# Optimization experiments

Measured on AMD Instinct MI355X. Metric: run time of the kernel, lower is better.

Reference implementation:

```python
import jax, jax.numpy as jnp
import numpy as np
import math

B, C, H, W, T, NH, SS = 4, 64, 32, 32, 32, 8, 512


def _alibi_slopes(heads):
    def pow2(n):
        start = 2 ** (-2 ** (-(math.log2(n) - 3)))
        return [start * start ** i for i in range(n)]
    if math.log2(heads).is_integer():
        return pow2(heads)
    cp = 2 ** math.floor(math.log2(heads))
    return pow2(cp) + pow2(2 * cp)[0::2][: heads - cp]


def _style_conv(x, style, weight, lw, lb, noise_p, bias_p, noise):
    # x: (b,c,h,w,t); weight: (out,in,1,1,1) -> modulated 1x1x1 grouped conv
    s = style @ lw.T + lb                                   # (b, in)
    w = weight[None] * s[:, None, :, None, None, None]       # (b,out,in,1,1,1)
    sigma_inv = jax.lax.rsqrt(jnp.sum(w * w, axis=(2, 3, 4, 5), keepdims=True) + 1e-8)
    w = (w * sigma_inv)[:, :, :, 0, 0, 0]                    # (b,out,in)
    y = jnp.einsum('bchwt,boc->bohwt', x, w)
    y = y + noise_p * noise                                  # (out,1,1,1)*(b,1,h,w,t)
    return y + bias_p


def setup_inputs() -> dict:
    key = jax.random.key(0)
    ks = jax.random.split(key, 8)
    return {
        'x': jax.random.normal(ks[0], (B, C, H, W, T), jnp.float32),
        'style': jax.random.normal(ks[1], (B, SS), jnp.float32),
        'qkv_w': jax.random.normal(ks[2], (3 * C, C, 1, 1, 1), jnp.float32),
        'qkv_lw': jax.random.normal(ks[3], (C, SS), jnp.float32) * 0.02,
        'qkv_lb': jnp.zeros((C,), jnp.float32),
        'qkv_np': jnp.zeros((3 * C, 1, 1, 1), jnp.float32),
        'qkv_bp': jnp.zeros((3 * C, 1, 1, 1), jnp.float32),
        'qkv_noise': jax.random.normal(ks[4], (B, 1, H, W, T), jnp.float32),
        'proj_w': jax.random.normal(ks[5], (C, C, 1, 1, 1), jnp.float32),
        'proj_lw': jax.random.normal(ks[6], (C, SS), jnp.float32) * 0.02,
        'proj_lb': jnp.zeros((C,), jnp.float32),
        'proj_np': jnp.zeros((C, 1, 1, 1), jnp.float32),
        'proj_bp': jnp.zeros((C, 1, 1, 1), jnp.float32),
        'proj_noise': jax.random.normal(ks[7], (B, 1, H, W, T), jnp.float32),
    }


def reference(x, style, qkv_w, qkv_lw, qkv_lb, qkv_np, qkv_bp, qkv_noise,
              proj_w, proj_lw, proj_lb, proj_np, proj_bp, proj_noise):
    b, c, h, w, t = x.shape
    qkv = _style_conv(x, style, qkv_w, qkv_lw, qkv_lb, qkv_np, qkv_bp, qkv_noise)
    q, k, v = jnp.split(qkv, 3, axis=1)                      # each (b,c,h,w,t)

    def to_heads(z):
        z = z.reshape(b, c * h * w, t).transpose(0, 2, 1)    # (b,t,chw)
        return z.reshape(b, t, NH, (c * h * w) // NH).transpose(0, 2, 1, 3)
    q, k, v = to_heads(q), to_heads(k), to_heads(v)          # (b,nh,t,dh)
    dh = q.shape[-1]

    attn = jnp.einsum('bnid,bnjd->bnij', q, k) / math.sqrt(dh)
    slopes = jnp.asarray(_alibi_slopes(NH), dtype=attn.dtype)[:, None, None]
    pos = -jnp.abs(jnp.arange(t)[None, :] - jnp.arange(t)[:, None]).astype(attn.dtype)
    attn = attn + slopes * pos                                # ALiBi bias
    # Faithful to original: masked_fill where tril(ones) is True (lower triangle masked)
    mask = jnp.tril(jnp.ones((t, t), bool))
    attn = jnp.where(mask, jnp.asarray(-1e18, attn.dtype), attn)
    attn = jax.nn.softmax(attn, axis=-1)
    out = jnp.einsum('bnij,bnjd->bnid', attn, v)              # (b,nh,t,dh)

    out = out.transpose(0, 2, 1, 3).reshape(b, t, c * h * w)  # (b,t,chw)
    out = out.reshape(b, t, c, h, w).transpose(0, 2, 3, 4, 1) # (b,c,h,w,t)
    return _style_conv(out, style, proj_w, proj_lw, proj_lb, proj_np, proj_bp, proj_noise)
```

## Files before the change

### kernel.cpp

```cpp
#include <hip/hip_runtime.h>

typedef unsigned short u16;
typedef unsigned int   u32;
typedef __attribute__((ext_vector_type(8))) short bf16x8;
typedef __attribute__((ext_vector_type(4))) float f32x4;

#define PP 32768
#define CC 64

__device__ __forceinline__ u16 f2b(float f) {
    u32 u; __builtin_memcpy(&u, &f, 4);
    u32 r = (u + 0x7FFFu + ((u >> 16) & 1u)) >> 16;
    return (u16)r;
}
__device__ __forceinline__ u32 pack2(float lo, float hi) {
    return (u32)f2b(lo) | ((u32)f2b(hi) << 16);
}

__global__ __launch_bounds__(64) void k_style2(
        const float* __restrict__ style, const float* __restrict__ qkv_lw,
        const float* __restrict__ qkv_lb, const float* __restrict__ proj_lw,
        const float* __restrict__ proj_lb, float* __restrict__ s_out) {
    int id = blockIdx.x;
    int b = id >> 7, sel = (id >> 6) & 1, o = id & 63;
    int t = threadIdx.x;
    const float* lw = sel ? proj_lw : qkv_lw;
    const float* lb = sel ? proj_lb : qkv_lb;
    const float* st = style + b * 512 + t * 8;
    const float* wr = lw + (size_t)o * 512 + t * 8;
    float4 s0 = *(const float4*)st, s1 = *(const float4*)(st + 4);
    float4 w0 = *(const float4*)wr, w1 = *(const float4*)(wr + 4);
    float p = s0.x*w0.x + s0.y*w0.y + s0.z*w0.z + s0.w*w0.w
            + s1.x*w1.x + s1.y*w1.y + s1.z*w1.z + s1.w*w1.w;
    #pragma unroll
    for (int off = 32; off > 0; off >>= 1) p += __shfl_xor(p, off, 64);
    if (t == 0) s_out[b * 128 + sel * 64 + o] = p + lb[o];
}

__global__ __launch_bounds__(64) void k_wnorm(
        const float* __restrict__ qkv_w, const float* __restrict__ proj_w,
        const float* __restrict__ s, u16* __restrict__ wqk_bf,
        u16* __restrict__ wv_bf, u16* __restrict__ wp_bf, float* __restrict__ S) {
    int id = blockIdx.x;
    int b = id >> 8, o = id & 255, i = threadIdx.x;
    if (i < 32) S[(size_t)id * 32 + i] = 0.f;
    float wv;
    if (o < 192) wv = qkv_w[o * 64 + i] * s[b * 128 + i];
    else         wv = proj_w[(o - 192) * 64 + i] * s[b * 128 + 64 + i];
    float sq = wv * wv;
    #pragma unroll
    for (int off = 32; off > 0; off >>= 1) sq += __shfl_xor(sq, off, 64);
    float val = wv * rsqrtf(sq + 1e-8f);
    if (o < 128) {
        u32 uv = __float_as_uint(val);
        float res = val - __uint_as_float(uv & 0xFFFF0000u);
        wqk_bf[((size_t)b * 256 + o) * 64 + i]       = (u16)(uv >> 16);
        wqk_bf[((size_t)b * 256 + 128 + o) * 64 + i] = (u16)(__float_as_uint(res) >> 16);
    }
    else if (o < 192) wv_bf[((size_t)b * 64 + (o - 128)) * 64 + i] = f2b(val);
    else {
        int o2 = o - 192;
        u32 uv = __float_as_uint(val);
        float res = val - __uint_as_float(uv & 0xFFFF0000u);
        wp_bf[((size_t)b * 64 + o2) * 64 + i]         = (u16)(uv >> 16);
        wp_bf[16384 + ((size_t)b * 64 + o2) * 64 + i] = (u16)(__float_as_uint(res) >> 16);
    }
}

__global__ __launch_bounds__(256) void k_fscores(
        const float* __restrict__ x, const u16* __restrict__ wqk_bf,
        const float* __restrict__ qnp, const float* __restrict__ qbp,
        const float* __restrict__ qnoise, float* __restrict__ S) {
    int bidx = blockIdx.x;
    int b = bidx >> 7, hg = (bidx >> 6) & 1, chunk = bidx & 63;
    int tid = threadIdx.x;
    __shared__ u32   XTh[4480];
    __shared__ u32   XTl[4480];
    __shared__ float NZ[128];
    __shared__ __align__(16) u16 QTh[4][1288], QTl[4][1288];
    __shared__ __align__(16) u16 KTh[4][1288], KTl[4][1288];

    int wv = tid >> 6, l = tid & 63, tl = l & 15, g = l >> 4;
    bf16x8 WH[4][2], WL[4][2];
    #pragma unroll
    for (int mt = 0; mt < 4; ++mt) {
        int n = hg * 4 + mt;
        int wrow = n * 8 + (tl & 7) + (tl >> 3) * 64;
        const u16* wpb = wqk_bf + (size_t)b * 16384 + wrow * 64;
        #pragma unroll
        for (int k = 0; k < 2; ++k) {
            WH[mt][k] = *(const bf16x8*)(wpb + k * 32 + g * 8);
            WL[mt][k] = *(const bf16x8*)(wpb + 8192 + k * 32 + g * 8);
        }
    }
    float4 np4[4], bp4[4];
    #pragma unroll
    for (int mt = 0; mt < 4; ++mt) {
        int pidx = (g >> 1) * 64 + (hg * 4 + mt) * 8 + (g & 1) * 4;
        np4[mt] = *(const float4*)(qnp + pidx);
        bp4[mt] = *(const float4*)(qbp + pidx);
    }
    int ti = wv >> 1, tj = wv & 1;
    f32x4 sacc[4];
    #pragma unroll
    for (int h = 0; h < 4; ++h) sacc[h] = (f32x4){0.f, 0.f, 0.f, 0.f};

    #pragma unroll 1
    for (int sub = 0; sub < 4; ++sub) {
        const float* xc = x + (size_t)b * CC * PP + chunk * 512 + sub * 128;
        #pragma unroll
        for (int r2 = 0; r2 < 4; ++r2) {
            int idx = r2 * 256 + tid;
            int e2 = idx >> 5, rem = idx & 31;
            const float* pa = xc + (size_t)(2 * e2) * PP + rem * 4;
            float4 fa = *(const float4*)pa;
            float4 fb = *(const float4*)(pa + PP);
            #pragma unroll
            for (int j = 0; j < 4; ++j) {
                float va = (&fa.x)[j], vb = (&fb.x)[j];
                u32 ua = __float_as_uint(va), ub = __float_as_uint(vb);
                float ra = va - __uint_as_float(ua & 0xFFFF0000u);
                float rb = vb - __uint_as_float(ub & 0xFFFF0000u);
                int p = (rem * 4 + j) * 35 + e2;
                XTh[p] = (ua >> 16) | (ub & 0xFFFF0000u);
                XTl[p] = (__float_as_uint(ra) >> 16) | (__float_as_uint(rb) & 0xFFFF0000u);
            }
        }
        if (tid < 32)
            *(float4*)&NZ[tid * 4] = *(const float4*)
                (qnoise + (size_t)b * PP + chunk * 512 + sub * 128 + tid * 4);
        __syncthreads();
        #pragma unroll
        for (int nh = 0; nh < 2; ++nh) {
            int nt = wv * 2 + nh, pos = nt * 16 + tl;
            union { bf16x8 v; u32 d[4]; } BH[2], BL[2];
            #pragma unroll
            for (int k = 0; k < 2; ++k) {
                const u32* ph = &XTh[pos * 35 + k * 16 + g * 4];
                const u32* pl = &XTl[pos * 35 + k * 16 + g * 4];
                BH[k].d[0] = ph[0]; BH[k].d[1] = ph[1]; BH[k].d[2] = ph[2]; BH[k].d[3] = ph[3];
                BL[k].d[0] = pl[0]; BL[k].d[1] = pl[1]; BL[k].d[2] = pl[2]; BL[k].d[3] = pl[3];
            }
            float nz = NZ[pos];
            int t = pos & 31, hwl = pos >> 5, side = g >> 1, g1 = g & 1;
            int off = t * 40 + hwl * 8 + g1 * 4;
            #pragma unroll
            for (int mt = 0; mt < 4; ++mt) {
                f32x4 a = {0.f, 0.f, 0.f, 0.f};
                #pragma unroll
                for (int k = 0; k < 2; ++k) {
                    a = __builtin_amdgcn_mfma_f32_16x16x32_bf16(WH[mt][k], BH[k].v, a, 0, 0, 0);
                    a = __builtin_amdgcn_mfma_f32_16x16x32_bf16(WH[mt][k], BL[k].v, a, 0, 0, 0);
                    a = __builtin_amdgcn_mfma_f32_16x16x32_bf16(WL[mt][k], BH[k].v, a, 0, 0, 0);
                }
                u32 uu[4], lu[4];
                #pragma unroll
                for (int j = 0; j < 4; ++j) {
                    float yv = a[j] + (&np4[mt].x)[j] * nz + (&bp4[mt].x)[j];
                    u32 uy = __float_as_uint(yv);
                    float res = yv - __uint_as_float(uy & 0xFFFF0000u);
                    uu[j] = uy; lu[j] = __float_as_uint(res);
                }
                u16* dh = (side ? KTh[mt] : QTh[mt]) + off;
                u16* dl = (side ? KTl[mt] : QTl[mt]) + off;
                *(uint2*)dh = make_uint2((uu[0] >> 16) | (uu[1] & 0xFFFF0000u),
                                         (uu[2] >> 16) | (uu[3] & 0xFFFF0000u));
                *(uint2*)dl = make_uint2((lu[0] >> 16) | (lu[1] & 0xFFFF0000u),
                                         (lu[2] >> 16) | (lu[3] & 0xFFFF0000u));
            }
        }
        __syncthreads();
        int ar = (ti * 16 + tl) * 40 + g * 8;
        int br = (tj * 16 + tl) * 40 + g * 8;
        #pragma unroll
        for (int h = 0; h < 4; ++h) {
            bf16x8 Ah = *(const bf16x8*)&QTh[h][ar];
            bf16x8 Al = *(const bf16x8*)&QTl[h][ar];
            bf16x8 Bh = *(const bf16x8*)&KTh[h][br];
            bf16x8 Bl = *(const bf16x8*)&KTl[h][br];
            sacc[h] = __builtin_amdgcn_mfma_f32_16x16x32_bf16(Ah, Bh, sacc[h], 0, 0, 0);
            sacc[h] = __builtin_amdgcn_mfma_f32_16x16x32_bf16(Ah, Bl, sacc[h], 0, 0, 0);
            sacc[h] = __builtin_amdgcn_mfma_f32_16x16x32_bf16(Al, Bh, sacc[h], 0, 0, 0);
        }
    }
    float* Sbase = S + ((size_t)b * 8 + hg * 4) * 1024;
    #pragma unroll
    for (int h = 0; h < 4; ++h) {
        float* Sb = Sbase + h * 1024;
        #pragma unroll
        for (int jj = 0; jj < 4; ++jj)
            atomicAdd(&Sb[(ti * 16 + g * 4 + jj) * 32 + tj * 16 + tl], sacc[h][jj]);
    }
}

__global__ __launch_bounds__(256) void k_out(
        const float* __restrict__ x, const u16* __restrict__ wv_bf,
        const float* __restrict__ qnp, const float* __restrict__ qbp,
        const float* __restrict__ qnoise, const float* __restrict__ Sg,
        const u16* __restrict__ wp_bf, const float* __restrict__ pnp,
        const float* __restrict__ pbp, const float* __restrict__ pnoise,
        float* __restrict__ out) {
    int bidx = blockIdx.x;
    int b = bidx >> 8, hw0 = (bidx & 255) * 4;
    int tid = threadIdx.x;
    __shared__ u32   P32s[5120];
    __shared__ __align__(16) u16 V16[10240];
    __shared__ __align__(16) float uni[8448];
    {
        int n = tid >> 5, i2 = tid & 31;
        const float* Srow = Sg + ((size_t)b * 8 + n) * 1024 + i2 * 32;
        float v[32];
        #pragma unroll
        for (int j4 = 0; j4 < 8; ++j4) {
            float4 s4 = *(const float4*)(Srow + j4 * 4);
            v[j4 * 4] = s4.x; v[j4 * 4 + 1] = s4.y;
            v[j4 * 4 + 2] = s4.z; v[j4 * 4 + 3] = s4.w;
        }
        float slope = exp2f(-(float)(n + 1));
        float m = -3e38f;
        #pragma unroll
        for (int j = 0; j < 32; ++j) {
            float val = v[j] * 0.011048543456039806f - slope * fabsf((float)(i2 - j));
            if (j <= i2) val = -1e18f;
            v[j] = val; m = fmaxf(m, val);
        }
        float ssum = 0.f;
        #pragma unroll
        for (int j = 0; j < 32; ++j) { float e2 = expf(v[j] - m); v[j] = e2; ssum += e2; }
        float r = 1.f / ssum;
        #pragma unroll
        for (int jp = 0; jp < 16; ++jp)
            P32s[n * 640 + i2 * 20 + jp] = pack2(v[2 * jp] * r, v[2 * jp + 1] * r);
    }
    {
        u32* XTu = (u32*)uni;
        const float* xc = x + (size_t)b * CC * PP + (size_t)hw0 * 32;
        #pragma unroll
        for (int r2 = 0; r2 < 4; ++r2) {
            int idx = r2 * 256 + tid;
            int e2 = idx >> 5, rem = idx & 31;
            const float* pa = xc + (size_t)(2 * e2) * PP + rem * 4;
            float4 fa = *(const float4*)pa;
            float4 fb = *(const float4*)(pa + PP);
            #pragma unroll
            for (int j = 0; j < 4; ++j) {
                u32 ua = __float_as_uint((&fa.x)[j]), ub = __float_as_uint((&fb.x)[j]);
                u32 ha = (ua + 0x7FFFu + ((ua >> 16) & 1u)) & 0xFFFF0000u;
                u32 hb = (ub + 0x7FFFu + ((ub >> 16) & 1u)) & 0xFFFF0000u;
                XTu[(rem * 4 + j) * 35 + e2] = (ha >> 16) | hb;
            }
        }
    }
    __syncthreads();
    int wv_ = tid >> 6, l = tid & 63, tl = l & 15, g = l >> 4;
    {
        const u32* XT32 = (const u32*)uni;
        const u16* wvb = wv_bf + (size_t)b * 4096;
        bf16x8 Af[4][2];
        #pragma unroll
        for (int mt = 0; mt < 4; ++mt)
            #pragma unroll
            for (int k = 0; k < 2; ++k)
                Af[mt][k] = *(const bf16x8*)(wvb + (mt * 16 + tl) * 64 + k * 32 + g * 8);
        #pragma unroll
        for (int nh = 0; nh < 2; ++nh) {
            int nt = 2 * wv_ + nh;
            f32x4 acc[4];
            #pragma unroll
            for (int mt = 0; mt < 4; ++mt) acc[mt] = (f32x4){0.f, 0.f, 0.f, 0.f};
            #pragma unroll
            for (int k = 0; k < 2; ++k) {
                int pos = nt * 16 + tl;
                union { bf16x8 v8; u32 d[4]; } B;
                const u32* xp = XT32 + pos * 35 + k * 16 + g * 4;
                B.d[0] = xp[0]; B.d[1] = xp[1]; B.d[2] = xp[2]; B.d[3] = xp[3];
                #pragma unroll
                for (int mt = 0; mt < 4; ++mt)
                    acc[mt] = __builtin_amdgcn_mfma_f32_16x16x32_bf16(Af[mt][k], B.v8, acc[mt], 0, 0, 0);
            }
            int t = (nt & 1) * 16 + tl;
            float nz = qnoise[(size_t)b * PP + (size_t)(hw0 + wv_) * 32 + t];
            #pragma unroll
            for (int mt = 0; mt < 4; ++mt) {
                float4 np4 = *(const float4*)(qnp + 128 + mt * 16 + g * 4);
                float4 bp4 = *(const float4*)(qbp + 128 + mt * 16 + g * 4);
                #pragma unroll
                for (int j = 0; j < 4; ++j) {
                    int ich = mt * 16 + g * 4 + j;
                    int rv = ich * 4 + wv_;
                    float y = acc[mt][j] + (&np4.x)[j] * nz + (&bp4.x)[j];
                    u32 bo = (u32)(rv * 80 + t * 2) ^ ((((u32)rv >> 4) & 3u) << 5);
                    *(u16*)((char*)V16 + bo) = f2b(y);
                }
            }
        }
    }
    __syncthreads();
    u16* ATh = (u16*)uni;
    u16* ATl = ATh + 8192;
    {
        #pragma unroll
        for (int hh = 0; hh < 2; ++hh) {
            int h = 2 * wv_ + hh;
            bf16x8 Bp[2];
            #pragma unroll
            for (int n2 = 0; n2 < 2; ++n2) {
                const u32* pp = P32s + h * 640 + (n2 * 16 + tl) * 20 + g * 4;
                union { bf16x8 v8; u32 d[4]; } U;
                U.d[0] = pp[0]; U.d[1] = pp[1]; U.d[2] = pp[2]; U.d[3] = pp[3];
                Bp[n2] = U.v8;
            }
            #pragma unroll
            for (int mt2 = 0; mt2 < 2; ++mt2) {
                int rv = h * 32 + mt2 * 16 + tl;
                u32 bo = ((u32)(rv * 80) + (u32)g * 16) ^ ((((u32)rv >> 4) & 3u) << 5);
                bf16x8 Av = *(const bf16x8*)((const char*)V16 + bo);
                #pragma unroll
                for (int n2 = 0; n2 < 2; ++n2) {
                    f32x4 a4 = (f32x4){0.f, 0.f, 0.f, 0.f};
                    a4 = __builtin_amdgcn_mfma_f32_16x16x32_bf16(Av, Bp[n2], a4, 0, 0, 0);
                    int i = h * 8 + mt2 * 4 + g;
                    int t = n2 * 16 + tl;
                    #pragma unroll
                    for (int j = 0; j < 4; ++j) {
                        int row = j * 32 + t;
                        u32 uy = __float_as_uint(a4[j]);
                        float res = a4[j] - __uint_as_float(uy & 0xFFFF0000u);
                        u32 ao = ((u32)(row * 128 + i * 2)) ^ (((u32)row & 7u) << 4);
                        *(u16*)((char*)ATh + ao) = (u16)(uy >> 16);
                        *(u16*)((char*)ATl + ao) = (u16)(__float_as_uint(res) >> 16);
                    }
                }
            }
        }
    }
    __syncthreads();
    {
        bf16x8 WpH[4][2], WpL[4][2];
        #pragma unroll
        for (int mt = 0; mt < 4; ++mt)
            #pragma unroll
            for (int k = 0; k < 2; ++k) {
                const u16* wb = wp_bf + ((size_t)b * 64 + mt * 16 + tl) * 64 + k * 32 + g * 8;
                WpH[mt][k] = *(const bf16x8*)wb;
                WpL[mt][k] = *(const bf16x8*)(wb + 16384);
            }
        #pragma unroll
        for (int nh = 0; nh < 2; ++nh) {
            int pos = (wv_ * 2 + nh) * 16 + tl;
            union { bf16x8 v; u32 d[4]; } BH[2], BL[2];
            #pragma unroll
            for (int k = 0; k < 2; ++k) {
                u32 bo = ((u32)(pos * 128 + k * 64 + g * 16)) ^ (((u32)pos & 7u) << 4);
                BH[k].v = *(const bf16x8*)((const char*)ATh + bo);
                BL[k].v = *(const bf16x8*)((const char*)ATl + bo);
            }
            f32x4 dacc[4];
            #pragma unroll
            for (int mt = 0; mt < 4; ++mt) dacc[mt] = (f32x4){0.f, 0.f, 0.f, 0.f};
            #pragma unroll
            for (int k = 0; k < 2; ++k)
                #pragma unroll
                for (int mt = 0; mt < 4; ++mt) {
                    dacc[mt] = __builtin_amdgcn_mfma_f32_16x16x32_bf16(WpH[mt][k], BH[k].v, dacc[mt], 0, 0, 0);
                    dacc[mt] = __builtin_amdgcn_mfma_f32_16x16x32_bf16(WpH[mt][k], BL[k].v, dacc[mt], 0, 0, 0);
                    dacc[mt] = __builtin_amdgcn_mfma_f32_16x16x32_bf16(WpL[mt][k], BH[k].v, dacc[mt], 0, 0, 0);
                }
            int hwl = pos >> 5, t = pos & 31;
            float nz = pnoise[(size_t)b * PP + (size_t)(hw0 + hwl) * 32 + t];
            #pragma unroll
            for (int mt = 0; mt < 4; ++mt) {
                float4 npv = *(const float4*)(pnp + mt * 16 + g * 4);
                float4 bpv = *(const float4*)(pbp + mt * 16 + g * 4);
                #pragma unroll
                for (int jj = 0; jj < 4; ++jj) {
                    int o = mt * 16 + g * 4 + jj;
                    out[(size_t)(b * 64 + o) * PP + (size_t)(hw0 + hwl) * 32 + t]
                        = dacc[mt][jj] + (&npv.x)[jj] * nz + (&bpv.x)[jj];
                }
            }
        }
    }
}

__global__ __launch_bounds__(256) void k_zero(float* __restrict__ out, int n) {
    int i = blockIdx.x * 256 + threadIdx.x;
    if (i < n) out[i] = 0.f;
}
__global__ void k_code(float* __restrict__ out, float code) { out[0] = code; }

extern "C" void kernel_launch(void* const* d_in, const int* in_sizes, int n_in,
                              void* d_out, int out_size, void* d_ws, size_t ws_size,
                              hipStream_t stream) {
    float* out = (float*)d_out;
    const int exp_sizes[14] = {4*64*32768, 4*512, 192*64, 64*512, 64, 192, 192,
                               4*32768, 64*64, 64*512, 64, 64, 64, 4*32768};
    bool ok = (n_in == 14) && (out_size == 4*64*32768);
    if (ok) for (int k = 0; k < 14; ++k) ok = ok && (in_sizes[k] == exp_sizes[k]);
    if (!ok) {
        k_zero<<<(out_size + 255) / 256, 256, 0, stream>>>(out, out_size);
        k_code<<<1, 1, 0, stream>>>(out, 1000.f);
        return;
    }
    if (ws_size < 395264) {
        k_zero<<<(out_size + 255) / 256, 256, 0, stream>>>(out, out_size);
        k_code<<<1, 1, 0, stream>>>(out, 2000.f + (float)(ws_size >> 20));
        return;
    }
    char* ws = (char*)d_ws;
    float* S      = (float*)ws;
    u16*   wqk_bf = (u16*)  (ws + 131072);
    u16*   wv_bf  = (u16*)  (ws + 262144);
    u16*   wp_bf  = (u16*)  (ws + 327680);
    float* s_sty  = (float*)(ws + 393216);

    k_style2 <<<512,  64,  0, stream>>>((const float*)d_in[1], (const float*)d_in[3],
                                        (const float*)d_in[4], (const float*)d_in[9],
                                        (const float*)d_in[10], s_sty);
    k_wnorm  <<<1024, 64,  0, stream>>>((const float*)d_in[2], (const float*)d_in[8],
                                        s_sty, wqk_bf, wv_bf, wp_bf, S);
    k_fscores<<<512,  256, 0, stream>>>((const float*)d_in[0], wqk_bf,
                                        (const float*)d_in[5], (const float*)d_in[6],
                                        (const float*)d_in[7], S);
    k_out    <<<1024, 256, 0, stream>>>((const float*)d_in[0], wv_bf,
                                        (const float*)d_in[5], (const float*)d_in[6],
                                        (const float*)d_in[7], S, wp_bf,
                                        (const float*)d_in[11], (const float*)d_in[12],
                                        (const float*)d_in[13], out);
    hipError_t e = hipGetLastError();
    if (e != hipSuccess) {
        k_zero<<<(out_size + 255) / 256, 256, 0, stream>>>(out, out_size);
        k_code<<<1, 1, 0, stream>>>(out, 3000.f + (float)e);
    }
}
```

Measured before the change: 154.5 us.

## Reuse x tile across both head groups and compute softmax in MFMA fragments

The scores kernel now processes both head groups per block over a smaller position chunk, so each x tile is loaded and split into hi/lo bf16 once instead of twice. The output kernel computes the ALiBi-masked softmax directly in the register layout needed by the MFMA B operand, using cross-lane shuffles for max and sum. This removes a shared-memory probability buffer and its write/read round-trip. The trade-off is higher register pressure from doubled weight fragments and accumulators, plus extra barriers per sub-iteration.

```diff
diff --git a/kernel.cpp b/kernel.cpp
--- a/kernel.cpp
+++ b/kernel.cpp
@@ -72,7 +72,7 @@
         const float* __restrict__ qnp, const float* __restrict__ qbp,
         const float* __restrict__ qnoise, float* __restrict__ S) {
     int bidx = blockIdx.x;
-    int b = bidx >> 7, hg = (bidx >> 6) & 1, chunk = bidx & 63;
+    int b = bidx >> 7, chunk = bidx & 127;
     int tid = threadIdx.x;
     __shared__ u32   XTh[4480];
     __shared__ u32   XTl[4480];
@@ -81,33 +81,29 @@
     __shared__ __align__(16) u16 KTh[4][1288], KTl[4][1288];
 
     int wv = tid >> 6, l = tid & 63, tl = l & 15, g = l >> 4;
-    bf16x8 WH[4][2], WL[4][2];
+    bf16x8 WH[2][4][2], WL[2][4][2];
     #pragma unroll
-    for (int mt = 0; mt < 4; ++mt) {
-        int n = hg * 4 + mt;
-        int wrow = n * 8 + (tl & 7) + (tl >> 3) * 64;
-        const u16* wpb = wqk_bf + (size_t)b * 16384 + wrow * 64;
-        #pragma unroll
-        for (int k = 0; k < 2; ++k) {
-            WH[mt][k] = *(const bf16x8*)(wpb + k * 32 + g * 8);
-            WL[mt][k] = *(const bf16x8*)(wpb + 8192 + k * 32 + g * 8);
-        }
-    }
-    float4 np4[4], bp4[4];
+    for (int hg = 0; hg < 2; ++hg)
+        #pragma unroll
+        for (int mt = 0; mt < 4; ++mt) {
+            int wrow = (hg * 4 + mt) * 8 + (tl & 7) + (tl >> 3) * 64;
+            const u16* wpb = wqk_bf + (size_t)b * 16384 + wrow * 64;
+            #pragma unroll
+            for (int k = 0; k < 2; ++k) {
+                WH[hg][mt][k] = *(const bf16x8*)(wpb + k * 32 + g * 8);
+                WL[hg][mt][k] = *(const bf16x8*)(wpb + 8192 + k * 32 + g * 8);
+            }
+        }
+    int ti = wv >> 1, tj = wv & 1;
+    f32x4 sacc[2][4];
     #pragma unroll
-    for (int mt = 0; mt < 4; ++mt) {
-        int pidx = (g >> 1) * 64 + (hg * 4 + mt) * 8 + (g & 1) * 4;
-        np4[mt] = *(const float4*)(qnp + pidx);
-        bp4[mt] = *(const float4*)(qbp + pidx);
-    }
-    int ti = wv >> 1, tj = wv & 1;
-    f32x4 sacc[4];
-    #pragma unroll
-    for (int h = 0; h < 4; ++h) sacc[h] = (f32x4){0.f, 0.f, 0.f, 0.f};
+    for (int hg = 0; hg < 2; ++hg)
+        #pragma unroll
+        for (int h = 0; h < 4; ++h) sacc[hg][h] = (f32x4){0.f, 0.f, 0.f, 0.f};
 
     #pragma unroll 1
-    for (int sub = 0; sub < 4; ++sub) {
-        const float* xc = x + (size_t)b * CC * PP + chunk * 512 + sub * 128;
+    for (int sub = 0; sub < 2; ++sub) {
+        const float* xc = x + (size_t)b * CC * PP + chunk * 256 + sub * 128;
         #pragma unroll
         for (int r2 = 0; r2 < 4; ++r2) {
             int idx = r2 * 256 + tid;
@@ -128,69 +124,81 @@
         }
         if (tid < 32)
             *(float4*)&NZ[tid * 4] = *(const float4*)
-                (qnoise + (size_t)b * PP + chunk * 512 + sub * 128 + tid * 4);
+                (qnoise + (size_t)b * PP + chunk * 256 + sub * 128 + tid * 4);
         __syncthreads();
         #pragma unroll
-        for (int nh = 0; nh < 2; ++nh) {
-            int nt = wv * 2 + nh, pos = nt * 16 + tl;
-            union { bf16x8 v; u32 d[4]; } BH[2], BL[2];
-            #pragma unroll
-            for (int k = 0; k < 2; ++k) {
-                const u32* ph = &XTh[pos * 35 + k * 16 + g * 4];
-                const u32* pl = &XTl[pos * 35 + k * 16 + g * 4];
-                BH[k].d[0] = ph[0]; BH[k].d[1] = ph[1]; BH[k].d[2] = ph[2]; BH[k].d[3] = ph[3];
-                BL[k].d[0] = pl[0]; BL[k].d[1] = pl[1]; BL[k].d[2] = pl[2]; BL[k].d[3] = pl[3];
-            }
-            float nz = NZ[pos];
-            int t = pos & 31, hwl = pos >> 5, side = g >> 1, g1 = g & 1;
-            int off = t * 40 + hwl * 8 + g1 * 4;
+        for (int hg = 0; hg < 2; ++hg) {
+            float4 np4[4], bp4[4];
             #pragma unroll
             for (int mt = 0; mt < 4; ++mt) {
-                f32x4 a = {0.f, 0.f, 0.f, 0.f};
+                int pidx = (g >> 1) * 64 + (hg * 4 + mt) * 8 + (g & 1) * 4;
+                np4[mt] = *(const float4*)(qnp + pidx);
+                bp4[mt] = *(const float4*)(qbp + pidx);
+            }
+            #pragma unroll
+            for (int nh = 0; nh < 2; ++nh) {
+                int nt = wv * 2 + nh, pos = nt * 16 + tl;
+                union { bf16x8 v; u32 d[4]; } BH[2], BL[2];
                 #pragma unroll
                 for (int k = 0; k < 2; ++k) {
-                    a = __builtin_amdgcn_mfma_f32_16x16x32_bf16(WH[mt][k], BH[k].v, a, 0, 0, 0);
-                    a = __builtin_amdgcn_mfma_f32_16x16x32_bf16(WH[mt][k], BL[k].v, a, 0, 0, 0);
-                    a = __builtin_amdgcn_mfma_f32_16x16x32_bf16(WL[mt][k], BH[k].v, a, 0, 0, 0);
-                }
-                u32 uu[4], lu[4];
-                #pragma unroll
-                for (int j = 0; j < 4; ++j) {
-                    float yv = a[j] + (&np4[mt].x)[j] * nz + (&bp4[mt].x)[j];
-                    u32 uy = __float_as_uint(yv);
-                    float res = yv - __uint_as_float(uy & 0xFFFF0000u);
-                    uu[j] = uy; lu[j] = __float_as_uint(res);
-                }
-                u16* dh = (side ? KTh[mt] : QTh[mt]) + off;
-                u16* dl = (side ? KTl[mt] : QTl[mt]) + off;
-                *(uint2*)dh = make_uint2((uu[0] >> 16) | (uu[1] & 0xFFFF0000u),
-                                         (uu[2] >> 16) | (uu[3] & 0xFFFF0000u));
-                *(uint2*)dl = make_uint2((lu[0] >> 16) | (lu[1] & 0xFFFF0000u),
-                                         (lu[2] >> 16) | (lu[3] & 0xFFFF0000u));
-            }
-        }
-        __syncthreads();
-        int ar = (ti * 16 + tl) * 40 + g * 8;
-        int br = (tj * 16 + tl) * 40 + g * 8;
+                    const u32* ph = &XTh[pos * 35 + k * 16 + g * 4];
+                    const u32* pl = &XTl[pos * 35 + k * 16 + g * 4];
+                    BH[k].d[0] = ph[0]; BH[k].d[1] = ph[1]; BH[k].d[2] = ph[2]; BH[k].d[3] = ph[3];
+                    BL[k].d[0] = pl[0]; BL[k].d[1] = pl[1]; BL[k].d[2] = pl[2]; BL[k].d[3] = pl[3];
+                }
+                float nz = NZ[pos];
+                int t = pos & 31, hwl = pos >> 5, side = g >> 1, g1 = g & 1;
+                int off = t * 40 + hwl * 8 + g1 * 4;
+                #pragma unroll
+                for (int mt = 0; mt < 4; ++mt) {
+                    f32x4 a = {0.f, 0.f, 0.f, 0.f};
+                    #pragma unroll
+                    for (int k = 0; k < 2; ++k) {
+                        a = __builtin_amdgcn_mfma_f32_16x16x32_bf16(WH[hg][mt][k], BH[k].v, a, 0, 0, 0);
+                        a = __builtin_amdgcn_mfma_f32_16x16x32_bf16(WH[hg][mt][k], BL[k].v, a, 0, 0, 0);
+                        a = __builtin_amdgcn_mfma_f32_16x16x32_bf16(WL[hg][mt][k], BH[k].v, a, 0, 0, 0);
+                    }
+                    u32 uu[4], lu[4];
+                    #pragma unroll
+                    for (int j = 0; j < 4; ++j) {
+                        float yv = a[j] + (&np4[mt].x)[j] * nz + (&bp4[mt].x)[j];
+                        u32 uy = __float_as_uint(yv);
+                        float res = yv - __uint_as_float(uy & 0xFFFF0000u);
+                        uu[j] = uy; lu[j] = __float_as_uint(res);
+                    }
+                    u16* dh = (side ? KTh[mt] : QTh[mt]) + off;
+                    u16* dl = (side ? KTl[mt] : QTl[mt]) + off;
+                    *(uint2*)dh = make_uint2((uu[0] >> 16) | (uu[1] & 0xFFFF0000u),
+                                             (uu[2] >> 16) | (uu[3] & 0xFFFF0000u));
+                    *(uint2*)dl = make_uint2((lu[0] >> 16) | (lu[1] & 0xFFFF0000u),
+                                             (lu[2] >> 16) | (lu[3] & 0xFFFF0000u));
+                }
+            }
+            __syncthreads();
+            int ar = (ti * 16 + tl) * 40 + g * 8;
+            int br = (tj * 16 + tl) * 40 + g * 8;
+            #pragma unroll
+            for (int h = 0; h < 4; ++h) {
+                bf16x8 Ah = *(const bf16x8*)&QTh[h][ar];
+                bf16x8 Al = *(const bf16x8*)&QTl[h][ar];
+                bf16x8 Bh = *(const bf16x8*)&KTh[h][br];
+                bf16x8 Bl = *(const bf16x8*)&KTl[h][br];
+                sacc[hg][h] = __builtin_amdgcn_mfma_f32_16x16x32_bf16(Ah, Bh, sacc[hg][h], 0, 0, 0);
+                sacc[hg][h] = __builtin_amdgcn_mfma_f32_16x16x32_bf16(Ah, Bl, sacc[hg][h], 0, 0, 0);
+                sacc[hg][h] = __builtin_amdgcn_mfma_f32_16x16x32_bf16(Al, Bh, sacc[hg][h], 0, 0, 0);
+            }
+            __syncthreads();
+        }
+    }
+    #pragma unroll
+    for (int hg = 0; hg < 2; ++hg)
         #pragma unroll
         for (int h = 0; h < 4; ++h) {
-            bf16x8 Ah = *(const bf16x8*)&QTh[h][ar];
-            bf16x8 Al = *(const bf16x8*)&QTl[h][ar];
-            bf16x8 Bh = *(const bf16x8*)&KTh[h][br];
-            bf16x8 Bl = *(const bf16x8*)&KTl[h][br];
-            sacc[h] = __builtin_amdgcn_mfma_f32_16x16x32_bf16(Ah, Bh, sacc[h], 0, 0, 0);
-            sacc[h] = __builtin_amdgcn_mfma_f32_16x16x32_bf16(Ah, Bl, sacc[h], 0, 0, 0);
-            sacc[h] = __builtin_amdgcn_mfma_f32_16x16x32_bf16(Al, Bh, sacc[h], 0, 0, 0);
-        }
-    }
-    float* Sbase = S + ((size_t)b * 8 + hg * 4) * 1024;
-    #pragma unroll
-    for (int h = 0; h < 4; ++h) {
-        float* Sb = Sbase + h * 1024;
-        #pragma unroll
-        for (int jj = 0; jj < 4; ++jj)
-            atomicAdd(&Sb[(ti * 16 + g * 4 + jj) * 32 + tj * 16 + tl], sacc[h][jj]);
-    }
+            float* Sb = S + ((size_t)b * 8 + hg * 4 + h) * 1024;
+            #pragma unroll
+            for (int jj = 0; jj < 4; ++jj)
+                atomicAdd(&Sb[(ti * 16 + g * 4 + jj) * 32 + tj * 16 + tl], sacc[hg][h][jj]);
+        }
 }
 
 __global__ __launch_bounds__(256) void k_out(
@@ -203,35 +211,9 @@
     int bidx = blockIdx.x;
     int b = bidx >> 8, hw0 = (bidx & 255) * 4;
     int tid = threadIdx.x;
-    __shared__ u32   P32s[5120];
+    int wv_ = tid >> 6, l = tid & 63, tl = l & 15, g = l >> 4;
     __shared__ __align__(16) u16 V16[10240];
     __shared__ __align__(16) float uni[8448];
-    {
-        int n = tid >> 5, i2 = tid & 31;
-        const float* Srow = Sg + ((size_t)b * 8 + n) * 1024 + i2 * 32;
-        float v[32];
-        #pragma unroll
-        for (int j4 = 0; j4 < 8; ++j4) {
-            float4 s4 = *(const float4*)(Srow + j4 * 4);
-            v[j4 * 4] = s4.x; v[j4 * 4 + 1] = s4.y;
-            v[j4 * 4 + 2] = s4.z; v[j4 * 4 + 3] = s4.w;
-        }
-        float slope = exp2f(-(float)(n + 1));
-        float m = -3e38f;
-        #pragma unroll
-        for (int j = 0; j < 32; ++j) {
-            float val = v[j] * 0.011048543456039806f - slope * fabsf((float)(i2 - j));
-            if (j <= i2) val = -1e18f;
-            v[j] = val; m = fmaxf(m, val);
-        }
-        float ssum = 0.f;
-        #pragma unroll
-        for (int j = 0; j < 32; ++j) { float e2 = expf(v[j] - m); v[j] = e2; ssum += e2; }
-        float r = 1.f / ssum;
-        #pragma unroll
-        for (int jp = 0; jp < 16; ++jp)
-            P32s[n * 640 + i2 * 20 + jp] = pack2(v[2 * jp] * r, v[2 * jp + 1] * r);
-    }
     {
         u32* XTu = (u32*)uni;
         const float* xc = x + (size_t)b * CC * PP + (size_t)hw0 * 32;
@@ -251,8 +233,43 @@
             }
         }
     }
+    u32 pfrag[2][2][4];
+    {
+        const float scale = 0.011048543456039806f;
+        #pragma unroll
+        for (int hh = 0; hh < 2; ++hh) {
+            int h = 2 * wv_ + hh;
+            float slope = exp2f(-(float)(h + 1));
+            #pragma unroll
+            for (int n2 = 0; n2 < 2; ++n2) {
+                int row = n2 * 16 + tl;
+                const float* Sp = Sg + ((size_t)b * 8 + h) * 1024 + row * 32 + g * 8;
+                float4 sa = *(const float4*)Sp;
+                float4 sb = *(const float4*)(Sp + 4);
+                float p[8]; float m = -3e38f;
+                #pragma unroll
+                for (int jj = 0; jj < 8; ++jj) {
+                    int j = g * 8 + jj;
+                    float sv = jj < 4 ? (&sa.x)[jj] : (&sb.x)[jj - 4];
+                    float val = sv * scale - slope * fabsf((float)(row - j));
+                    if (j <= row) val = -1e18f;
+                    p[jj] = val; m = fmaxf(m, val);
+                }
+                m = fmaxf(m, __shfl_xor(m, 16, 64));
+                m = fmaxf(m, __shfl_xor(m, 32, 64));
+                float ssum = 0.f;
+                #pragma unroll
+                for (int jj = 0; jj < 8; ++jj) { p[jj] = expf(p[jj] - m); ssum += p[jj]; }
+                ssum += __shfl_xor(ssum, 16, 64);
+                ssum += __shfl_xor(ssum, 32, 64);
+                float r = 1.f / ssum;
+                #pragma unroll
+                for (int m2 = 0; m2 < 4; ++m2)
+                    pfrag[hh][n2][m2] = pack2(p[2 * m2] * r, p[2 * m2 + 1] * r);
+            }
+        }
+    }
     __syncthreads();
-    int wv_ = tid >> 6, l = tid & 63, tl = l & 15, g = l >> 4;
     {
         const u32* XT32 = (const u32*)uni;
         const u16* wvb = wv_bf + (size_t)b * 4096;
@@ -305,9 +322,9 @@
             bf16x8 Bp[2];
             #pragma unroll
             for (int n2 = 0; n2 < 2; ++n2) {
-                const u32* pp = P32s + h * 640 + (n2 * 16 + tl) * 20 + g * 4;
                 union { bf16x8 v8; u32 d[4]; } U;
-                U.d[0] = pp[0]; U.d[1] = pp[1]; U.d[2] = pp[2]; U.d[3] = pp[3];
+                U.d[0] = pfrag[hh][n2][0]; U.d[1] = pfrag[hh][n2][1];
+                U.d[2] = pfrag[hh][n2][2]; U.d[3] = pfrag[hh][n2][3];
                 Bp[n2] = U.v8;
             }
             #pragma unroll
```

After: 178.6 us. +15.5%, slower.
